# Kernel optimization log

Measured on AMD Instinct MI355X. Metric: run time of the kernel, lower is better.

The kernel has to match this reference:

```python
import jax, jax.numpy as jnp
import numpy as np
import math

D_MODEL = 1024
N_HEADS = 16
D_K = D_MODEL // N_HEADS
B, S = 4, 2048


def setup_inputs() -> dict:
    key = jax.random.key(0)
    ks = jax.random.split(key, 11)
    std = 1.0 / math.sqrt(D_MODEL)
    inp = {
        "query": jax.random.normal(ks[0], (B, S, D_MODEL), dtype=jnp.float32),
        "key_in": jax.random.normal(ks[1], (B, S, D_MODEL), dtype=jnp.float32),
        "value": jax.random.normal(ks[2], (B, S, D_MODEL), dtype=jnp.float32),
        "Wq": jax.random.normal(ks[3], (D_MODEL, D_MODEL), dtype=jnp.float32) * std,
        "bq": jnp.zeros((D_MODEL,), dtype=jnp.float32),
        "Wk": jax.random.normal(ks[4], (D_MODEL, D_MODEL), dtype=jnp.float32) * std,
        "bk": jnp.zeros((D_MODEL,), dtype=jnp.float32),
        "Wv": jax.random.normal(ks[5], (D_MODEL, D_MODEL), dtype=jnp.float32) * std,
        "bv": jnp.zeros((D_MODEL,), dtype=jnp.float32),
        "Wo": jax.random.normal(ks[6], (D_MODEL, D_MODEL), dtype=jnp.float32) * std,
        "bo": jnp.zeros((D_MODEL,), dtype=jnp.float32),
    }
    return inp


def reference(query, key_in, value, Wq, bq, Wk, bk, Wv, bv, Wo, bo):
    b, s, _ = query.shape
    scale = math.sqrt(D_K)
    # projections: nn.Linear computes x @ W.T + b
    Q = (query @ Wq.T + bq).reshape(b, s, N_HEADS, D_K).transpose(0, 2, 1, 3)
    K = (key_in @ Wk.T + bk).reshape(b, s, N_HEADS, D_K).transpose(0, 2, 1, 3)
    V = (value @ Wv.T + bv).reshape(b, s, N_HEADS, D_K).transpose(0, 2, 1, 3)
    # [b, h, s, s]
    scores = jnp.einsum("bhqd,bhkd->bhqk", Q, K) / scale
    causal = jnp.tril(jnp.ones((s, s), dtype=bool))
    scores = jnp.where(causal[None, None, :, :], scores, jnp.float32(-1e9))
    attn = jax.nn.softmax(scores, axis=-1)
    out = jnp.einsum("bhqk,bhkd->bhqd", attn, V)
    out = out.transpose(0, 2, 1, 3).reshape(b, s, D_MODEL)
    return out @ Wo.T + bo
```

## Files before the change

kernel.cpp:

```cpp
#include <hip/hip_runtime.h>
#include <hip/hip_bf16.h>
#include <cstdint>

#define DM   1024
#define NH   16
#define DKK  64
#define BB   4
#define SS   2048

typedef __attribute__((ext_vector_type(8)))  short short8;
typedef __attribute__((ext_vector_type(4)))  float f32x4;
typedef __attribute__((ext_vector_type(16))) float f32x16;

__device__ __forceinline__ unsigned short f2bf(float f) {
    union { float f; uint32_t u; } v; v.f = f;
    uint32_t u = v.u;
    uint32_t r = (u + 0x7FFFu + ((u >> 16) & 1u)) >> 16;
    return (unsigned short)r;
}

#define GLL(src, dst) __builtin_amdgcn_global_load_lds(                      \
        (__attribute__((address_space(1))) void*)(src),                      \
        (__attribute__((address_space(3))) void*)(dst), 16, 0, 0)

__global__ void cvt_all(const float* __restrict__ q, const float* __restrict__ k,
                        const float* __restrict__ v,
                        const float* __restrict__ wq, const float* __restrict__ wk,
                        const float* __restrict__ wv, const float* __restrict__ wo,
                        unsigned short* __restrict__ dact, unsigned short* __restrict__ dw)
{
    int i = blockIdx.x * 256 + threadIdx.x;
    const float* s;
    unsigned short* d;
    if (i < 3145728) {
        int a = i >> 20, r = i & 1048575;
        int j = r >> 7, kb = r & 127;
        int kbs = (kb & ~7) | ((kb ^ j) & 7);
        s = (a == 0 ? q : a == 1 ? k : v) + (size_t)j * 1024 + kbs * 8;
        d = dact + ((size_t)a << 23) + (size_t)j * 1024 + kb * 8;
    } else {
        int t = i - 3145728;
        int a = t >> 17, r = t & 131071;
        int j = r >> 7, kb = r & 127;
        int kbs = (kb & ~7) | ((kb ^ j) & 7);
        s = (a == 0 ? wq : a == 1 ? wk : a == 2 ? wv : wo) + (size_t)j * 1024 + kbs * 8;
        d = dw + ((size_t)a << 20) + (size_t)j * 1024 + kb * 8;
    }
    float4 f0 = *(const float4*)(s);
    float4 f1 = *(const float4*)(s + 4);
    union { uint32_t u[4]; short8 s8; } c;
    asm("v_cvt_pk_bf16_f32 %0, %1, %2" : "=v"(c.u[0]) : "v"(f0.x), "v"(f0.y));
    asm("v_cvt_pk_bf16_f32 %0, %1, %2" : "=v"(c.u[1]) : "v"(f0.z), "v"(f0.w));
    asm("v_cvt_pk_bf16_f32 %0, %1, %2" : "=v"(c.u[2]) : "v"(f1.x), "v"(f1.y));
    asm("v_cvt_pk_bf16_f32 %0, %1, %2" : "=v"(c.u[3]) : "v"(f1.z), "v"(f1.w));
    *(short8*)d = c.s8;
}

__global__ __launch_bounds__(512, 2) void gemm_qkv(
        const unsigned short* __restrict__ Act,
        const unsigned short* __restrict__ Wq, const unsigned short* __restrict__ Wk,
        const unsigned short* __restrict__ Wv,
        const float* __restrict__ bq, const float* __restrict__ bk, const float* __restrict__ bv,
        unsigned short* __restrict__ Qo, unsigned short* __restrict__ Ko,
        unsigned short* __restrict__ Vo, const float qscale)
{
    const int orig = blockIdx.x;
    const int wid  = (orig & 7) * 48 + (orig >> 3);
    const int z    = wid >> 7;
    const int r    = wid & 127;
    const int brow = (r >> 2) * 256;
    const int bcol = (r & 3) * 256;

    const unsigned short* A  = Act + ((size_t)z << 23);
    const unsigned short* Bw = (z == 0) ? Wq : (z == 1) ? Wk : Wv;
    const float* bias        = (z == 0) ? bq : (z == 1) ? bk : bv;

    __shared__ __align__(16) unsigned short lA[3][2][8192];
    __shared__ __align__(16) unsigned short lB[2][2][8192];

    const int tid = threadIdx.x;
    const int w = tid >> 6, l = tid & 63;
    const int wm = w >> 2, wn = w & 3;
    const int lrow = l & 15, hi = l >> 4;

    const unsigned short* Asrc = A  + (size_t)(brow + (tid >> 3)) * 1024 + (tid & 7) * 8;
    const unsigned short* Bsrc = Bw + (size_t)(bcol + (tid >> 3)) * 1024 + (tid & 7) * 8;

    int axr[2];
    axr[0] = ((hi ^ (lrow & 7)) << 4);
    axr[1] = (((4 + hi) ^ (lrow & 7)) << 4);

    short8 bfr[4][2];
    f32x4 acc[8][4] = {};

#define STG_A(KT, H)                                                                         \
    { GLL(Asrc + (size_t)((H) * 128) * 1024 + (KT) * 64,      &lA[(KT) % 3][H][w * 512]);    \
      GLL(Asrc + (size_t)((H) * 128 + 64) * 1024 + (KT) * 64, &lA[(KT) % 3][H][4096 + w * 512]); }
#define STG_B(KT, H)                                                                         \
    { GLL(Bsrc + (size_t)((H) * 128) * 1024 + (KT) * 64,      &lB[(KT) & 1][H][w * 512]);    \
      GLL(Bsrc + (size_t)((H) * 128 + 64) * 1024 + (KT) * 64, &lB[(KT) & 1][H][4096 + w * 512]); }
#define VM8 asm volatile("s_waitcnt vmcnt(8)" ::: "memory")
#define VM0 asm volatile("s_waitcnt vmcnt(0)" ::: "memory")

#define PH(KT, MQ, READB, STG, WAIT)                                                         \
    {                                                                                        \
        const char* la_ = (const char*)lA[(KT) % 3][wm];                                     \
        const char* lb_ = (const char*)lB[(KT) & 1][wn >> 1];                                \
        if (READB) {                                                                         \
            _Pragma("unroll") for (int n = 0; n < 4; ++n)                                    \
            _Pragma("unroll") for (int kk = 0; kk < 2; ++kk)                                 \
                bfr[n][kk] = *(const short8*)(lb_ + ((wn & 1) * 64 + n * 16 + lrow) * 128 + axr[kk]); \
        }                                                                                    \
        short8 af_[2][2];                                                                    \
        _Pragma("unroll") for (int j = 0; j < 2; ++j)                                        \
        _Pragma("unroll") for (int kk = 0; kk < 2; ++kk)                                     \
            af_[j][kk] = *(const short8*)(la_ + (((MQ) * 2 + j) * 16 + lrow) * 128 + axr[kk]); \
        STG;                                                                                 \
        WAIT;                                                                                \
        __builtin_amdgcn_s_barrier();                                                        \
        asm volatile("s_waitcnt lgkmcnt(0)" ::: "memory");                                   \
        __builtin_amdgcn_sched_barrier(0);                                                   \
        __builtin_amdgcn_s_setprio(1);                                                       \
        _Pragma("unroll") for (int j = 0; j < 2; ++j)                                        \
        _Pragma("unroll") for (int n = 0; n < 4; ++n)                                        \
        _Pragma("unroll") for (int kk = 0; kk < 2; ++kk)                                     \
            acc[(MQ) * 2 + j][n] = __builtin_amdgcn_mfma_f32_16x16x32_bf16(                  \
                af_[j][kk], bfr[n][kk], acc[(MQ) * 2 + j][n], 0, 0, 0);                      \
        __builtin_amdgcn_s_setprio(0);                                                       \
        __builtin_amdgcn_s_barrier();                                                        \
    }

    STG_A(0, 0); STG_A(0, 1); STG_B(0, 0); STG_B(0, 1);
    STG_A(1, 0); STG_A(1, 1); STG_B(1, 0); STG_B(1, 1);
    VM8;
    __builtin_amdgcn_s_barrier();

    for (int i = 0; i < 7; ++i) {
        const int kt = 2 * i;
        PH(kt,     0, 1, STG_A(kt + 2, 0), (void)0);
        PH(kt,     1, 0, STG_A(kt + 2, 1), (void)0);
        PH(kt,     2, 0, STG_B(kt + 2, 0), (void)0);
        PH(kt,     3, 0, STG_B(kt + 2, 1), VM8);
        PH(kt + 1, 0, 1, STG_A(kt + 3, 0), (void)0);
        PH(kt + 1, 1, 0, STG_A(kt + 3, 1), (void)0);
        PH(kt + 1, 2, 0, STG_B(kt + 3, 0), (void)0);
        PH(kt + 1, 3, 0, STG_B(kt + 3, 1), VM8);
    }
    PH(14, 0, 1, (void)0, (void)0);
    PH(14, 1, 0, (void)0, (void)0);
    PH(14, 2, 0, (void)0, (void)0);
    PH(14, 3, 0, (void)0, VM0);
    PH(15, 0, 1, (void)0, (void)0);
    PH(15, 1, 0, (void)0, (void)0);
    PH(15, 2, 0, (void)0, (void)0);
    PH(15, 3, 0, (void)0, (void)0);

#undef PH
#undef STG_A
#undef STG_B

    const float ascale = (z == 0) ? qscale : 1.0f;
#pragma unroll
    for (int m = 0; m < 8; ++m) {
#pragma unroll
        for (int n = 0; n < 4; ++n) {
            const int i0 = brow + wm * 128 + m * 16 + hi * 4;
            const int j  = bcol + wn * 64 + n * 16 + lrow;
            const float bj = bias[j];
            const int hh = j >> 6, d = j & 63;
            if (z < 2) {
                unsigned short* Cb = (z == 0) ? Qo : Ko;
#pragma unroll
                for (int t = 0; t < 4; ++t) {
                    const int i = i0 + t;
                    const int b = i >> 11, s = i & 2047;
                    Cb[(((size_t)(b * NH + hh) * SS) + s) * DKK + d] = f2bf((acc[m][n][t] + bj) * ascale);
                }
            } else {
                const int b = i0 >> 11, s0 = i0 & 2047;
                ushort4 pk;
                pk.x = f2bf(acc[m][n][0] + bj);
                pk.y = f2bf(acc[m][n][1] + bj);
                pk.z = f2bf(acc[m][n][2] + bj);
                pk.w = f2bf(acc[m][n][3] + bj);
                *(ushort4*)(Vo + (((size_t)(b * NH + hh) * DKK) + d) * SS + s0) = pk;
            }
        }
    }
}

__global__ __launch_bounds__(256) void gemm_out(
        const unsigned short* __restrict__ A,
        const unsigned short* __restrict__ Bw,
        const float* __restrict__ bias,
        float* __restrict__ Cout)
{
    const int orig = blockIdx.y * 8 + blockIdx.x;
    const int wid  = (orig & 7) * 64 + (orig >> 3);
    const int brow = (wid >> 3) * 128;
    const int bcol = (wid & 7) * 128;

    __shared__ __align__(16) unsigned short lA[128 * 64];
    __shared__ __align__(16) unsigned short lB[2][128 * 64];

    const int tid = threadIdx.x;
    const int w = tid >> 6, l = tid & 63;
    const int wr = (w >> 1) * 64, wc = (w & 1) * 64;
    const int lrow = l & 15;
    const int hi = l >> 4;
    const int sr = l >> 3, scb = l & 7;

    const unsigned short* aga[4];
    const unsigned short* bga[4];
    int awb[4], lbo[4];
#pragma unroll
    for (int i = 0; i < 4; ++i) {
        const int chunk = w * 4 + i;
        const int r = chunk * 8 + sr;
        aga[i] = A  + (size_t)(brow + r) * 1024 + scb * 8;
        bga[i] = Bw + (size_t)(bcol + r) * 1024 + scb * 8;
        awb[i] = chunk * 1024 + sr * 128 + ((scb ^ sr) << 4);
        lbo[i] = chunk * 512;
    }

    short8 aX[4], aY[4];
    f32x4 acc[4][4] = {};

#pragma unroll
    for (int i = 0; i < 4; ++i) GLL(bga[i], lB[0] + lbo[i]);
#pragma unroll
    for (int i = 0; i < 4; ++i) aX[i] = *(const short8*)(aga[i]);
#pragma unroll
    for (int i = 0; i < 4; ++i) aY[i] = *(const short8*)(aga[i] + 64);

#define OUT_WR(CUR)                                                     \
    _Pragma("unroll")                                                   \
    for (int i = 0; i < 4; ++i)                                         \
        *(short8*)((char*)lA + awb[i]) = CUR[i];

#define OUT_MFMA(LB)                                                                              \
    {                                                                                             \
        const unsigned short* lb = (LB);                                                          \
        __builtin_amdgcn_s_setprio(1);                                                            \
        _Pragma("unroll")                                                                         \
        for (int kk = 0; kk < 2; ++kk) {                                                          \
            short8 af[4], bf[4];                                                                  \
            _Pragma("unroll")                                                                     \
            for (int m = 0; m < 4; ++m) {                                                         \
                const int row = wr + m * 16 + lrow;                                               \
                const int pb = (kk * 4 + hi) ^ (row & 7);                                         \
                af[m] = *(const short8*)((const char*)lA + row * 128 + (pb << 4));                \
            }                                                                                     \
            _Pragma("unroll")                                                                     \
            for (int n = 0; n < 4; ++n) {                                                         \
                const int row = wc + n * 16 + lrow;                                               \
                const int pb = (kk * 4 + hi) ^ (row & 7);                                         \
                bf[n] = *(const short8*)((const char*)lb + row * 128 + (pb << 4));                \
            }                                                                                     \
            _Pragma("unroll")                                                                     \
            for (int m = 0; m < 4; ++m)                                                           \
                _Pragma("unroll")                                                                 \
                for (int n = 0; n < 4; ++n)                                                       \
                    acc[m][n] = __builtin_amdgcn_mfma_f32_16x16x32_bf16(af[m], bf[n], acc[m][n], 0, 0, 0); \
        }                                                                                         \
        __builtin_amdgcn_s_setprio(0);                                                            \
    }

    for (int t = 0; t < 14; t += 2) {
        OUT_WR(aX);
        {
            const int ko = (t + 2) * 64;
#pragma unroll
            for (int i = 0; i < 4; ++i) aX[i] = *(const short8*)(aga[i] + ko);
            const int kb = (t + 1) * 64;
#pragma unroll
            for (int i = 0; i < 4; ++i) GLL(bga[i] + kb, lB[1] + lbo[i]);
        }
        asm volatile("s_waitcnt vmcnt(8) lgkmcnt(0)" ::: "memory");
        __builtin_amdgcn_s_barrier();
        OUT_MFMA(lB[0]);
        asm volatile("" ::: "memory");
        __builtin_amdgcn_s_barrier();

        OUT_WR(aY);
        {
            const int ko = (t + 3) * 64;
#pragma unroll
            for (int i = 0; i < 4; ++i) aY[i] = *(const short8*)(aga[i] + ko);
            const int kb = (t + 2) * 64;
#pragma unroll
            for (int i = 0; i < 4; ++i) GLL(bga[i] + kb, lB[0] + lbo[i]);
        }
        asm volatile("s_waitcnt vmcnt(8) lgkmcnt(0)" ::: "memory");
        __builtin_amdgcn_s_barrier();
        OUT_MFMA(lB[1]);
        asm volatile("" ::: "memory");
        __builtin_amdgcn_s_barrier();
    }
    OUT_WR(aX);
#pragma unroll
    for (int i = 0; i < 4; ++i) GLL(bga[i] + 15 * 64, lB[1] + lbo[i]);
    asm volatile("s_waitcnt vmcnt(4) lgkmcnt(0)" ::: "memory");
    __builtin_amdgcn_s_barrier();
    OUT_MFMA(lB[0]);
    asm volatile("" ::: "memory");
    __builtin_amdgcn_s_barrier();
    OUT_WR(aY);
    asm volatile("s_waitcnt vmcnt(0) lgkmcnt(0)" ::: "memory");
    __builtin_amdgcn_s_barrier();
    OUT_MFMA(lB[1]);

#pragma unroll
    for (int m = 0; m < 4; ++m) {
#pragma unroll
        for (int n = 0; n < 4; ++n) {
            const int i0 = brow + wr + m * 16 + (l >> 4) * 4;
            const int j  = bcol + wc + n * 16 + lrow;
            const float bj = bias[j];
#pragma unroll
            for (int t = 0; t < 4; ++t)
                Cout[(size_t)(i0 + t) * DM + j] = acc[m][n][t] + bj;
        }
    }
#undef OUT_WR
#undef OUT_MFMA
}

__global__ __launch_bounds__(256) void attn_kernel(
        const unsigned short* __restrict__ Q,
        const unsigned short* __restrict__ K,
        const unsigned short* __restrict__ Vt,
        unsigned short* __restrict__ AO)
{
    const int flat = blockIdx.y * 16 + blockIdx.x;
    const int r8 = flat & 7, k8 = flat >> 3;
    const int bh = r8 * 8 + (k8 & 7);
    const int qchunk = 15 - (k8 >> 3);
    const int tid = threadIdx.x;
    const int w = tid >> 6, l = tid & 63;
    const int ln = l & 31, h = l >> 5;
    const int qb = qchunk * 128;
    const int q0w = qb + w * 32;

    __shared__ __align__(16) char lK[2][4096];
    __shared__ __align__(16) char lV[2][4096];

    const unsigned short* Qp = Q  + ((size_t)bh * SS + q0w) * DKK;
    const unsigned short* Kp = K  + (size_t)bh * SS * DKK;
    const unsigned short* Vp = Vt + (size_t)bh * DKK * SS;

    const int srow = tid >> 3, scb = tid & 7;
    const int swb = srow * 128 + ((scb * 16) ^ ((srow & 7) << 4));
    const unsigned short* ksrc = Kp + srow * DKK + scb * 8;
    const int vd = (scb < 4) ? srow : (srow + 32);
    const unsigned short* vsrc = Vp + (size_t)vd * SS + (scb & 3) * 8;

    int ka[4], va[4];
#pragma unroll
    for (int ks = 0; ks < 4; ++ks)
        ka[ks] = ln * 128 + ((ks * 32 + h * 16) ^ ((ln & 7) << 4));
#pragma unroll
    for (int c = 0; c < 4; ++c)
        va[c] = ln * 128 + ((c * 32 + h * 16) ^ ((ln & 7) << 4));

    short8 qf[4];
#pragma unroll
    for (int ks = 0; ks < 4; ++ks)
        qf[ks] = *(const short8*)(Qp + (size_t)ln * DKK + ks * 16 + h * 8);

    f32x16 o0 = {}, o1 = {};
    float lsum = 0.f;

    const int Tc = qb / 32;
    const int NT = Tc + 4;

    auto compute = [&](int t, int buf) {
        const char* kb = lK[buf];
        const char* vb = lV[buf];
        short8 kf[4];
#pragma unroll
        for (int ks = 0; ks < 4; ++ks) kf[ks] = *(const short8*)(kb + ka[ks]);

        f32x16 s = {};
        __builtin_amdgcn_s_setprio(1);
#pragma unroll
        for (int ks = 0; ks < 4; ++ks)
            s = __builtin_amdgcn_mfma_f32_32x32x16_bf16(kf[ks], qf[ks], s, 0, 0, 0);
        __builtin_amdgcn_s_setprio(0);

        const bool diag = (t == Tc + w);
#pragma unroll
        for (int r = 0; r < 16; ++r) {
            float e;
            asm("v_exp_f32 %0, %1" : "=v"(e) : "v"(s[r]));
            if (diag) {
                const int crow = (r & 3) + 8 * (r >> 2) + 4 * h;
                e = (crow > ln) ? 0.f : e;
            }
            s[r] = e;
            lsum += e;
        }

        uint32_t pk[8];
#pragma unroll
        for (int i = 0; i < 8; ++i) {
            uint32_t d;
            asm("v_cvt_pk_bf16_f32 %0, %1, %2" : "=v"(d) : "v"(s[2 * i]), "v"(s[2 * i + 1]));
            pk[i] = d;
        }
        asm("v_permlane32_swap_b32 %0, %1" : "+v"(pk[0]), "+v"(pk[2]));
        asm("v_permlane32_swap_b32 %0, %1" : "+v"(pk[1]), "+v"(pk[3]));
        asm("v_permlane32_swap_b32 %0, %1" : "+v"(pk[4]), "+v"(pk[6]));
        asm("v_permlane32_swap_b32 %0, %1" : "+v"(pk[5]), "+v"(pk[7]));

        union Ux { uint32_t u[4]; short8 s8; } pa0, pa1;
        pa0.u[0] = pk[0]; pa0.u[1] = pk[1]; pa0.u[2] = pk[2]; pa0.u[3] = pk[3];
        pa1.u[0] = pk[4]; pa1.u[1] = pk[5]; pa1.u[2] = pk[6]; pa1.u[3] = pk[7];

        short8 vf00 = *(const short8*)(vb + va[0]);
        short8 vf10 = *(const short8*)(vb + va[1]);
        short8 vf01 = *(const short8*)(vb + va[2]);
        short8 vf11 = *(const short8*)(vb + va[3]);

        __builtin_amdgcn_s_setprio(1);
        o0 = __builtin_amdgcn_mfma_f32_32x32x16_bf16(pa0.s8, vf00, o0, 0, 0, 0);
        o0 = __builtin_amdgcn_mfma_f32_32x32x16_bf16(pa1.s8, vf10, o0, 0, 0, 0);
        o1 = __builtin_amdgcn_mfma_f32_32x32x16_bf16(pa0.s8, vf01, o1, 0, 0, 0);
        o1 = __builtin_amdgcn_mfma_f32_32x32x16_bf16(pa1.s8, vf11, o1, 0, 0, 0);
        __builtin_amdgcn_s_setprio(0);
    };

    short8 kA = *(const short8*)(ksrc);
    short8 vA = *(const short8*)(vsrc);
    *(short8*)(&lK[0][swb]) = kA;
    *(short8*)(&lV[0][swb]) = vA;
    kA = *(const short8*)(ksrc + 2048);
    vA = *(const short8*)(vsrc + 32);
    short8 kB = {}, vB = {};
    __syncthreads();

    int t = 0, buf = 0;
    for (;;) {
        if (t + 2 < NT) {
            kB = *(const short8*)(ksrc + (size_t)(t + 2) * 2048);
            vB = *(const short8*)(vsrc + (size_t)(t + 2) * 32);
        }
        if (t <= Tc + w) compute(t, buf);
        if (t + 1 < NT) {
            *(short8*)(&lK[buf ^ 1][swb]) = kA;
            *(short8*)(&lV[buf ^ 1][swb]) = vA;
        }
        __syncthreads();
        buf ^= 1;
        if (++t == NT) break;

        if (t + 2 < NT) {
            kA = *(const short8*)(ksrc + (size_t)(t + 2) * 2048);
            vA = *(const short8*)(vsrc + (size_t)(t + 2) * 32);
        }
        if (t <= Tc + w) compute(t, buf);
        if (t + 1 < NT) {
            *(short8*)(&lK[buf ^ 1][swb]) = kB;
            *(short8*)(&lV[buf ^ 1][swb]) = vB;
        }
        __syncthreads();
        buf ^= 1;
        if (++t == NT) break;
    }

    lsum += __shfl_xor(lsum, 32, 64);
    const float rcp = 1.0f / lsum;

    const int bb = bh >> 4, hh = bh & 15;
#pragma unroll
    for (int r = 0; r < 16; ++r) {
        const int crow = (r & 3) + 8 * (r >> 2) + 4 * h;
        const float rl = __shfl(rcp, crow, 64);
        const size_t row = (size_t)(bb * SS + q0w + crow) * DM + hh * DKK;
        AO[row + ln]      = f2bf(o0[r] * rl);
        AO[row + 32 + ln] = f2bf(o1[r] * rl);
    }
}

extern "C" void kernel_launch(void* const* d_in, const int* in_sizes, int n_in,
                              void* d_out, int out_size, void* d_ws, size_t ws_size,
                              hipStream_t stream)
{
    const float* query  = (const float*)d_in[0];
    const float* key_in = (const float*)d_in[1];
    const float* value  = (const float*)d_in[2];
    const float* Wq = (const float*)d_in[3];
    const float* bq = (const float*)d_in[4];
    const float* Wk = (const float*)d_in[5];
    const float* bk = (const float*)d_in[6];
    const float* Wv = (const float*)d_in[7];
    const float* bv = (const float*)d_in[8];
    const float* Wo = (const float*)d_in[9];
    const float* bo = (const float*)d_in[10];

    const size_t NACT = (size_t)BB * SS * DM;
    const size_t NWT  = (size_t)DM * DM;

    unsigned short* ws   = (unsigned short*)d_ws;
    unsigned short* actb = ws;
    unsigned short* wqb  = actb + 3 * NACT;
    unsigned short* wkb  = wqb + NWT;
    unsigned short* wvb  = wkb + NWT;
    unsigned short* wob  = wvb + NWT;
    unsigned short* Qb   = wob + NWT;
    unsigned short* Kb   = Qb + NACT;
    unsigned short* Vtb  = Kb + NACT;
    unsigned short* AOb  = Vtb + NACT;

    cvt_all<<<14336, 256, 0, stream>>>(query, key_in, value, Wq, Wk, Wv, Wo, actb, wqb);

    const float QSCALE = 0.125f * 1.44269504088896f;
    gemm_qkv<<<384, 512, 0, stream>>>(actb, wqb, wkb, wvb,
                                      bq, bk, bv, Qb, Kb, Vtb, QSCALE);

    attn_kernel<<<dim3(16, 64), 256, 0, stream>>>(Qb, Kb, Vtb, AOb);

    dim3 gg(DM / 128, (BB * SS) / 128);
    gemm_out<<<gg, 256, 0, stream>>>(AOb, wob, bo, (float*)d_out);
}
```

Measured before the change: 176.8 us.

## Fuse fp32-to-bf16 activation conversion into QKV GEMM, load fp32 tiles directly

Drops the separate activation conversion pass, so the QKV GEMM now streams fp32 activations straight into LDS with a swizzled layout and converts them to bf16 in registers before the MFMAs. The aim is to avoid writing and re-reading a bf16 copy of the three activation tensors, while the weights are still converted by a smaller kernel. In exchange the M tile shrinks from 256 to 128 rows to make room for fp32 LDS tiles, so the grid doubles to 768 blocks. Each A tile now costs twice the global and LDS bytes plus conversion ALU work, and each B tile is reused over fewer rows.

```diff
diff --git a/kernel.cpp b/kernel.cpp
--- a/kernel.cpp
+++ b/kernel.cpp
@@ -23,29 +23,16 @@
         (__attribute__((address_space(1))) void*)(src),                      \
         (__attribute__((address_space(3))) void*)(dst), 16, 0, 0)
 
-__global__ void cvt_all(const float* __restrict__ q, const float* __restrict__ k,
-                        const float* __restrict__ v,
-                        const float* __restrict__ wq, const float* __restrict__ wk,
-                        const float* __restrict__ wv, const float* __restrict__ wo,
-                        unsigned short* __restrict__ dact, unsigned short* __restrict__ dw)
+__global__ void cvt_w(const float* __restrict__ wq, const float* __restrict__ wk,
+                      const float* __restrict__ wv, const float* __restrict__ wo,
+                      unsigned short* __restrict__ dst)
 {
     int i = blockIdx.x * 256 + threadIdx.x;
-    const float* s;
-    unsigned short* d;
-    if (i < 3145728) {
-        int a = i >> 20, r = i & 1048575;
-        int j = r >> 7, kb = r & 127;
-        int kbs = (kb & ~7) | ((kb ^ j) & 7);
-        s = (a == 0 ? q : a == 1 ? k : v) + (size_t)j * 1024 + kbs * 8;
-        d = dact + ((size_t)a << 23) + (size_t)j * 1024 + kb * 8;
-    } else {
-        int t = i - 3145728;
-        int a = t >> 17, r = t & 131071;
-        int j = r >> 7, kb = r & 127;
-        int kbs = (kb & ~7) | ((kb ^ j) & 7);
-        s = (a == 0 ? wq : a == 1 ? wk : a == 2 ? wv : wo) + (size_t)j * 1024 + kbs * 8;
-        d = dw + ((size_t)a << 20) + (size_t)j * 1024 + kb * 8;
-    }
+    int a = i >> 17;
+    int r = i & 131071;
+    int j = r >> 7, kb = r & 127;
+    int kbs = (kb & ~7) | ((kb ^ j) & 7);
+    const float* s = (a == 0 ? wq : a == 1 ? wk : a == 2 ? wv : wo) + (size_t)j * 1024 + kbs * 8;
     float4 f0 = *(const float4*)(s);
     float4 f1 = *(const float4*)(s + 4);
     union { uint32_t u[4]; short8 s8; } c;
@@ -53,11 +40,11 @@
     asm("v_cvt_pk_bf16_f32 %0, %1, %2" : "=v"(c.u[1]) : "v"(f0.z), "v"(f0.w));
     asm("v_cvt_pk_bf16_f32 %0, %1, %2" : "=v"(c.u[2]) : "v"(f1.x), "v"(f1.y));
     asm("v_cvt_pk_bf16_f32 %0, %1, %2" : "=v"(c.u[3]) : "v"(f1.z), "v"(f1.w));
-    *(short8*)d = c.s8;
+    *(short8*)(dst + ((size_t)a << 20) + (size_t)j * 1024 + kb * 8) = c.s8;
 }
 
 __global__ __launch_bounds__(512, 2) void gemm_qkv(
-        const unsigned short* __restrict__ Act,
+        const float* __restrict__ Aq, const float* __restrict__ Ak, const float* __restrict__ Av,
         const unsigned short* __restrict__ Wq, const unsigned short* __restrict__ Wk,
         const unsigned short* __restrict__ Wv,
         const float* __restrict__ bq, const float* __restrict__ bk, const float* __restrict__ bv,
@@ -65,17 +52,17 @@
         unsigned short* __restrict__ Vo, const float qscale)
 {
     const int orig = blockIdx.x;
-    const int wid  = (orig & 7) * 48 + (orig >> 3);
-    const int z    = wid >> 7;
-    const int r    = wid & 127;
-    const int brow = (r >> 2) * 256;
-    const int bcol = (r & 3) * 256;
-
-    const unsigned short* A  = Act + ((size_t)z << 23);
+    const int wid  = (orig & 7) * 96 + (orig >> 3);
+    const int z    = wid >> 8;
+    const int rem  = wid & 255;
+    const int brow = (rem >> 2) * 128;
+    const int bcol = (rem & 3) * 256;
+
+    const float* Af          = (z == 0) ? Aq : (z == 1) ? Ak : Av;
     const unsigned short* Bw = (z == 0) ? Wq : (z == 1) ? Wk : Wv;
     const float* bias        = (z == 0) ? bq : (z == 1) ? bk : bv;
 
-    __shared__ __align__(16) unsigned short lA[3][2][8192];
+    __shared__ __align__(16) float          lAf[3][2][4096];
     __shared__ __align__(16) unsigned short lB[2][2][8192];
 
     const int tid = threadIdx.x;
@@ -83,7 +70,7 @@
     const int wm = w >> 2, wn = w & 3;
     const int lrow = l & 15, hi = l >> 4;
 
-    const unsigned short* Asrc = A  + (size_t)(brow + (tid >> 3)) * 1024 + (tid & 7) * 8;
+    const int asw = (tid >> 4) * 1024 + ((((tid >> 1) & 7) ^ ((tid >> 4) & 7)) << 3) + (tid & 1) * 4;
     const unsigned short* Bsrc = Bw + (size_t)(bcol + (tid >> 3)) * 1024 + (tid & 7) * 8;
 
     int axr[2];
@@ -91,43 +78,50 @@
     axr[1] = (((4 + hi) ^ (lrow & 7)) << 4);
 
     short8 bfr[4][2];
-    f32x4 acc[8][4] = {};
-
-#define STG_A(KT, H)                                                                         \
-    { GLL(Asrc + (size_t)((H) * 128) * 1024 + (KT) * 64,      &lA[(KT) % 3][H][w * 512]);    \
-      GLL(Asrc + (size_t)((H) * 128 + 64) * 1024 + (KT) * 64, &lA[(KT) % 3][H][4096 + w * 512]); }
-#define STG_B(KT, H)                                                                         \
-    { GLL(Bsrc + (size_t)((H) * 128) * 1024 + (KT) * 64,      &lB[(KT) & 1][H][w * 512]);    \
+    f32x4 acc[4][4] = {};
+
+#define STG_A(KT, H)                                                                           \
+    { GLL(Af + (size_t)(brow + (H) * 64 ) * 1024 + (KT) * 64 + asw, &lAf[(KT) % 3][H][w * 256]); \
+      GLL(Af + (size_t)(brow + (H) * 64 + 32) * 1024 + (KT) * 64 + asw, &lAf[(KT) % 3][H][2048 + w * 256]); }
+#define STG_B(KT, H)                                                                           \
+    { GLL(Bsrc + (size_t)((H) * 128) * 1024 + (KT) * 64,      &lB[(KT) & 1][H][w * 512]);      \
       GLL(Bsrc + (size_t)((H) * 128 + 64) * 1024 + (KT) * 64, &lB[(KT) & 1][H][4096 + w * 512]); }
 #define VM8 asm volatile("s_waitcnt vmcnt(8)" ::: "memory")
 #define VM0 asm volatile("s_waitcnt vmcnt(0)" ::: "memory")
 
-#define PH(KT, MQ, READB, STG, WAIT)                                                         \
-    {                                                                                        \
-        const char* la_ = (const char*)lA[(KT) % 3][wm];                                     \
-        const char* lb_ = (const char*)lB[(KT) & 1][wn >> 1];                                \
-        if (READB) {                                                                         \
-            _Pragma("unroll") for (int n = 0; n < 4; ++n)                                    \
-            _Pragma("unroll") for (int kk = 0; kk < 2; ++kk)                                 \
+#define PH(KT, MQ, READB, STG, WAIT)                                                           \
+    {                                                                                          \
+        const char* la_ = (const char*)lAf[(KT) % 3][wm];                                      \
+        const char* lb_ = (const char*)lB[(KT) & 1][wn >> 1];                                  \
+        if (READB) {                                                                           \
+            _Pragma("unroll") for (int n = 0; n < 4; ++n)                                      \
+            _Pragma("unroll") for (int kk = 0; kk < 2; ++kk)                                   \
                 bfr[n][kk] = *(const short8*)(lb_ + ((wn & 1) * 64 + n * 16 + lrow) * 128 + axr[kk]); \
-        }                                                                                    \
-        short8 af_[2][2];                                                                    \
-        _Pragma("unroll") for (int j = 0; j < 2; ++j)                                        \
-        _Pragma("unroll") for (int kk = 0; kk < 2; ++kk)                                     \
-            af_[j][kk] = *(const short8*)(la_ + (((MQ) * 2 + j) * 16 + lrow) * 128 + axr[kk]); \
-        STG;                                                                                 \
-        WAIT;                                                                                \
-        __builtin_amdgcn_s_barrier();                                                        \
-        asm volatile("s_waitcnt lgkmcnt(0)" ::: "memory");                                   \
-        __builtin_amdgcn_sched_barrier(0);                                                   \
-        __builtin_amdgcn_s_setprio(1);                                                       \
-        _Pragma("unroll") for (int j = 0; j < 2; ++j)                                        \
-        _Pragma("unroll") for (int n = 0; n < 4; ++n)                                        \
-        _Pragma("unroll") for (int kk = 0; kk < 2; ++kk)                                     \
-            acc[(MQ) * 2 + j][n] = __builtin_amdgcn_mfma_f32_16x16x32_bf16(                  \
-                af_[j][kk], bfr[n][kk], acc[(MQ) * 2 + j][n], 0, 0, 0);                      \
-        __builtin_amdgcn_s_setprio(0);                                                       \
-        __builtin_amdgcn_s_barrier();                                                        \
+        }                                                                                      \
+        short8 af_[2];                                                                         \
+        _Pragma("unroll") for (int kk = 0; kk < 2; ++kk) {                                     \
+            const int pb_ = (kk * 4 + hi) ^ (lrow & 7);                                        \
+            f32x4 lo_ = *(const f32x4*)(la_ + ((MQ) * 16 + lrow) * 256 + pb_ * 32);            \
+            f32x4 hf_ = *(const f32x4*)(la_ + ((MQ) * 16 + lrow) * 256 + pb_ * 32 + 16);       \
+            union { uint32_t u[4]; short8 s8; } c_;                                            \
+            asm("v_cvt_pk_bf16_f32 %0, %1, %2" : "=v"(c_.u[0]) : "v"(lo_[0]), "v"(lo_[1]));    \
+            asm("v_cvt_pk_bf16_f32 %0, %1, %2" : "=v"(c_.u[1]) : "v"(lo_[2]), "v"(lo_[3]));    \
+            asm("v_cvt_pk_bf16_f32 %0, %1, %2" : "=v"(c_.u[2]) : "v"(hf_[0]), "v"(hf_[1]));    \
+            asm("v_cvt_pk_bf16_f32 %0, %1, %2" : "=v"(c_.u[3]) : "v"(hf_[2]), "v"(hf_[3]));    \
+            af_[kk] = c_.s8;                                                                   \
+        }                                                                                      \
+        STG;                                                                                   \
+        WAIT;                                                                                  \
+        __builtin_amdgcn_s_barrier();                                                          \
+        asm volatile("s_waitcnt lgkmcnt(0)" ::: "memory");                                     \
+        __builtin_amdgcn_sched_barrier(0);                                                     \
+        __builtin_amdgcn_s_setprio(1);                                                         \
+        _Pragma("unroll") for (int n = 0; n < 4; ++n)                                          \
+        _Pragma("unroll") for (int kk = 0; kk < 2; ++kk)                                       \
+            acc[(MQ)][n] = __builtin_amdgcn_mfma_f32_16x16x32_bf16(                            \
+                af_[kk], bfr[n][kk], acc[(MQ)][n], 0, 0, 0);                                   \
+        __builtin_amdgcn_s_setprio(0);                                                         \
+        __builtin_amdgcn_s_barrier();                                                          \
     }
 
     STG_A(0, 0); STG_A(0, 1); STG_B(0, 0); STG_B(0, 1);
@@ -161,10 +155,10 @@
 
     const float ascale = (z == 0) ? qscale : 1.0f;
 #pragma unroll
-    for (int m = 0; m < 8; ++m) {
+    for (int m = 0; m < 4; ++m) {
 #pragma unroll
         for (int n = 0; n < 4; ++n) {
-            const int i0 = brow + wm * 128 + m * 16 + hi * 4;
+            const int i0 = brow + wm * 64 + m * 16 + hi * 4;
             const int j  = bcol + wn * 64 + n * 16 + lrow;
             const float bj = bias[j];
             const int hh = j >> 6, d = j & 63;
@@ -501,21 +495,20 @@
     const size_t NACT = (size_t)BB * SS * DM;
     const size_t NWT  = (size_t)DM * DM;
 
-    unsigned short* ws   = (unsigned short*)d_ws;
-    unsigned short* actb = ws;
-    unsigned short* wqb  = actb + 3 * NACT;
-    unsigned short* wkb  = wqb + NWT;
-    unsigned short* wvb  = wkb + NWT;
-    unsigned short* wob  = wvb + NWT;
-    unsigned short* Qb   = wob + NWT;
-    unsigned short* Kb   = Qb + NACT;
-    unsigned short* Vtb  = Kb + NACT;
-    unsigned short* AOb  = Vtb + NACT;
-
-    cvt_all<<<14336, 256, 0, stream>>>(query, key_in, value, Wq, Wk, Wv, Wo, actb, wqb);
+    unsigned short* ws  = (unsigned short*)d_ws;
+    unsigned short* wqb = ws;
+    unsigned short* wkb = wqb + NWT;
+    unsigned short* wvb = wkb + NWT;
+    unsigned short* wob = wvb + NWT;
+    unsigned short* Qb  = wob + NWT;
+    unsigned short* Kb  = Qb + NACT;
+    unsigned short* Vtb = Kb + NACT;
+    unsigned short* AOb = Vtb + NACT;
+
+    cvt_w<<<2048, 256, 0, stream>>>(Wq, Wk, Wv, Wo, ws);
 
     const float QSCALE = 0.125f * 1.44269504088896f;
-    gemm_qkv<<<384, 512, 0, stream>>>(actb, wqb, wkb, wvb,
+    gemm_qkv<<<768, 512, 0, stream>>>(query, key_in, value, wqb, wkb, wvb,
                                       bq, bk, bv, Qb, Kb, Vtb, QSCALE);
 
     attn_kernel<<<dim3(16, 64), 256, 0, stream>>>(Qb, Kb, Vtb, AOb);
```

New measurement: 179.3 us. No clear change (+1.4%).
